# Kernel tuning notes

Hardware: AMD Instinct MI355X
Metric: run time of the kernel (lower is better)

Reference implementation:

```python
import jax, jax.numpy as jnp
import numpy as np
from jax import lax

B, C, T = 64, 122, 500
COUT, D, H, FF, L = 64, 128, 8, 256, 2
NSUB, NCLS = 13, 4
EPS = 1e-5


def _gelu(x):
    return jax.nn.gelu(x, approximate=False)  # torch nn.GELU default (erf)


def _bn(x, g, b, m, v):
    # eval-mode BatchNorm1d over channel dim of [N, C, T]
    scale = (g / jnp.sqrt(v + EPS))[None, :, None]
    return (x - m[None, :, None]) * scale + b[None, :, None]


def _ln(x, g, b):
    mu = x.mean(-1, keepdims=True)
    var = ((x - mu) ** 2).mean(-1, keepdims=True)
    return (x - mu) / jnp.sqrt(var + EPS) * g + b


def _conv1d(x, w, b, pad):
    y = lax.conv_general_dilated(x, w, (1,), [(pad, pad)], dimension_numbers=('NCH', 'OIH', 'NCH'))
    return y + b[None, :, None]


def forward(x, subject_ids, conv1_w, conv1_b, bn1_g, bn1_b, bn1_m, bn1_v,
            conv2_w, conv2_b, bn2_g, bn2_b, bn2_m, bn2_v,
            proj_w, proj_b, elec_emb,
            qkv_w, qkv_b, out_w, out_b, ln1_g, ln1_b,
            ff1_w, ff1_b, ff2_w, ff2_b, ln2_g, ln2_b,
            heads_w, heads_b):
    bsz = x.shape[0]
    h = x.reshape(bsz * C, 1, T)                               # [B*C, 1, T]
    h = _gelu(_bn(_conv1d(h, conv1_w, conv1_b, 4), bn1_g, bn1_b, bn1_m, bn1_v))
    h = h.reshape(bsz * C, COUT, T // 2, 2).max(-1)            # MaxPool1d(2)
    h = _gelu(_bn(_conv1d(h, conv2_w, conv2_b, 2), bn2_g, bn2_b, bn2_m, bn2_v))
    h = h.mean(-1)                                             # AdaptiveAvgPool1d(1)
    tok = h @ proj_w.T + proj_b                                # [B*C, D]
    tok = tok.reshape(bsz, C, D) + elec_emb[:, :C, :]
    dh = D // H
    inv_sqrt_dh = 1.0 / float(np.sqrt(dh))
    for l in range(L):  # post-norm TransformerEncoderLayer, gelu activation
        qkv = jnp.einsum('bsd,ed->bse', tok, qkv_w[l]) + qkv_b[l]
        q, k, v = jnp.split(qkv, 3, axis=-1)
        q = q.reshape(bsz, C, H, dh)
        k = k.reshape(bsz, C, H, dh)
        v = v.reshape(bsz, C, H, dh)
        att = jax.nn.softmax(jnp.einsum('bqhd,bkhd->bhqk', q, k) * inv_sqrt_dh, axis=-1)
        ctx = jnp.einsum('bhqk,bkhd->bqhd', att, v).reshape(bsz, C, D)
        tok = _ln(tok + ctx @ out_w[l].T + out_b[l], ln1_g[l], ln1_b[l])
        ff = _gelu(tok @ ff1_w[l].T + ff1_b[l]) @ ff2_w[l].T + ff2_b[l]
        tok = _ln(tok + ff, ln2_g[l], ln2_b[l])
    pooled = tok.mean(axis=1)                                  # [B, D]
    # per-subject head routing == gather subject's weight/bias, batched matvec
    hw = heads_w[subject_ids]                                  # [B, NCLS, D]
    hb = heads_b[subject_ids]                                  # [B, NCLS]
    return jnp.einsum('bd,bcd->bc', pooled, hw) + hb


def setup_inputs() -> dict:
    key = jax.random.key(0)
    ks = jax.random.split(key, 16)
    def n(i, shape, s=0.02):
        return jax.random.normal(ks[i], shape, jnp.float32) * s
    return {
        'x': jax.random.normal(ks[0], (B, C, T), jnp.float32),
        'subject_ids': jax.random.randint(ks[1], (B,), 0, NSUB),
        'conv1_w': n(2, (COUT, 1, 9), 0.3), 'conv1_b': jnp.zeros((COUT,), jnp.float32),
        'bn1_g': jnp.ones((COUT,), jnp.float32), 'bn1_b': jnp.zeros((COUT,), jnp.float32),
        'bn1_m': jnp.zeros((COUT,), jnp.float32), 'bn1_v': jnp.ones((COUT,), jnp.float32),
        'conv2_w': n(3, (COUT, COUT, 5), 0.05), 'conv2_b': jnp.zeros((COUT,), jnp.float32),
        'bn2_g': jnp.ones((COUT,), jnp.float32), 'bn2_b': jnp.zeros((COUT,), jnp.float32),
        'bn2_m': jnp.zeros((COUT,), jnp.float32), 'bn2_v': jnp.ones((COUT,), jnp.float32),
        'proj_w': n(4, (D, COUT), 0.05), 'proj_b': jnp.zeros((D,), jnp.float32),
        'elec_emb': n(5, (1, C, D), 0.02),
        'qkv_w': n(6, (L, 3 * D, D), 0.05), 'qkv_b': jnp.zeros((L, 3 * D), jnp.float32),
        'out_w': n(7, (L, D, D), 0.05), 'out_b': jnp.zeros((L, D), jnp.float32),
        'ln1_g': jnp.ones((L, D), jnp.float32), 'ln1_b': jnp.zeros((L, D), jnp.float32),
        'ff1_w': n(8, (L, FF, D), 0.05), 'ff1_b': jnp.zeros((L, FF), jnp.float32),
        'ff2_w': n(9, (L, D, FF), 0.05), 'ff2_b': jnp.zeros((L, D), jnp.float32),
        'ln2_g': jnp.ones((L, D), jnp.float32), 'ln2_b': jnp.zeros((L, D), jnp.float32),
        'heads_w': n(10, (NSUB, NCLS, D), 0.05), 'heads_b': jnp.zeros((NSUB, NCLS), jnp.float32),
    }


def reference(x, subject_ids, conv1_w, conv1_b, bn1_g, bn1_b, bn1_m, bn1_v,
              conv2_w, conv2_b, bn2_g, bn2_b, bn2_m, bn2_v,
              proj_w, proj_b, elec_emb,
              qkv_w, qkv_b, out_w, out_b, ln1_g, ln1_b,
              ff1_w, ff1_b, ff2_w, ff2_b, ln2_g, ln2_b,
              heads_w, heads_b):
    return forward(x, subject_ids, conv1_w, conv1_b, bn1_g, bn1_b, bn1_m, bn1_v,
                   conv2_w, conv2_b, bn2_g, bn2_b, bn2_m, bn2_v,
                   proj_w, proj_b, elec_emb,
                   qkv_w, qkv_b, out_w, out_b, ln1_g, ln1_b,
                   ff1_w, ff1_b, ff2_w, ff2_b, ln2_g, ln2_b,
                   heads_w, heads_b)
```

## Files before the change

kernel.cpp:

```cpp
#include <hip/hip_runtime.h>
#include <math.h>

#define BB 64
#define CC 122
#define TT 500
#define NCOUT 64
#define DD 128
#define HHEADS 8
#define FFDIM 256
#define NLAYER 2
#define EPS 1e-5f
#define SEQ (BB*CC)

#define WS_W2T     0u
#define WS_S1      20480u
#define WS_SH1     20544u
#define WS_S2      20608u
#define WS_SH2     20672u
#define WS_WBF     20736u
#define WS_TOK     151808u
#define WS_QKV     1151232u
#define WS_CTX     4149504u
#define WS_GTAB    6148352u
#define WS_W1S     6149376u

#define WB_QKV  0u
#define WB_OUT  98304u
#define WB_FF1  131072u
#define WB_FF2  196608u

typedef __attribute__((ext_vector_type(8))) short bf16x8;
typedef __attribute__((ext_vector_type(4))) float f32x4;

__device__ __forceinline__ unsigned short f2bf(float f) {
    unsigned int u = __float_as_uint(f);
    unsigned int r = u + 0x7FFFu + ((u >> 16) & 1u);
    return (unsigned short)(r >> 16);
}

__device__ __forceinline__ float gelu_fast(float x) {
    float z = fabsf(x) * 0.70710678118654752f;
    float t = __builtin_amdgcn_rcpf(fmaf(0.3275911f, z, 1.0f));
    float p = fmaf(fmaf(fmaf(fmaf(1.061405429f, t, -1.453152027f), t,
                             1.421413741f), t, -0.284496736f), t, 0.254829592f);
    float e = __expf(-z * z);
    float erf_abs = fmaf(-p * t, e, 1.0f);
    float erf_x = copysignf(erf_abs, x);
    return 0.5f * x * (1.0f + erf_x);
}

__device__ __forceinline__ float gelu_tab(float x, const float* __restrict__ gt) {
    float p = fmaf(x, 32.0f, 256.0f);
    p = fminf(fmaxf(p, 0.0f), 511.999f);
    int i = (int)p;
    float fr = p - (float)i;
    float2 gd = *(const float2*)&gt[2*i];
    return fmaf(fr, gd.y, gd.x);
}

__global__ void prep_kernel(const float* __restrict__ conv1_w, const float* __restrict__ conv1_b,
                            const float* __restrict__ bn1_g, const float* __restrict__ bn1_b,
                            const float* __restrict__ bn1_m, const float* __restrict__ bn1_v,
                            const float* __restrict__ conv2_w, const float* __restrict__ conv2_b,
                            const float* __restrict__ bn2_g, const float* __restrict__ bn2_b,
                            const float* __restrict__ bn2_m, const float* __restrict__ bn2_v,
                            const float* __restrict__ qkv_w, const float* __restrict__ out_w,
                            const float* __restrict__ ff1_w, const float* __restrict__ ff2_w,
                            float* __restrict__ ws) {
    int idx = blockIdx.x * blockDim.x + threadIdx.x;
    if (idx < 20480) {
        int ci = idx & 63; int co = (idx >> 6) & 63; int kk = idx >> 12;
        unsigned short* wt = (unsigned short*)(ws + WS_W2T);
        wt[idx] = f2bf(conv2_w[(co*64 + ci)*5 + kk]);
    } else if (idx < 20544) {
        int i = idx - 20480;
        float s = bn1_g[i] * rsqrtf(bn1_v[i] + EPS);
        ws[WS_S1 + i] = s;
        ws[WS_SH1 + i] = (conv1_b[i] - bn1_m[i]) * s + bn1_b[i];
    } else if (idx < 20608) {
        int i = idx - 20544;
        float s = bn2_g[i] * rsqrtf(bn2_v[i] + EPS);
        ws[WS_S2 + i] = s;
        ws[WS_SH2 + i] = (conv2_b[i] - bn2_m[i]) * s + bn2_b[i];
    } else if (idx < 282752) {
        int r = idx - 20608;
        unsigned short* wbf = (unsigned short*)(ws + WS_WBF);
        float v;
        if (r < 98304)       v = qkv_w[r];
        else if (r < 131072) v = out_w[r - 98304];
        else if (r < 196608) v = ff1_w[r - 131072];
        else                 v = ff2_w[r - 196608];
        wbf[r] = f2bf(v);
    } else if (idx < 283264) {
        int i = idx - 282752;
        float x0 = (i - 256) * 0.03125f;
        float x1 = x0 + 0.03125f;
        float g0 = 0.5f*x0*(1.0f + erff(x0*0.70710678118654752f));
        float g1 = 0.5f*x1*(1.0f + erff(x1*0.70710678118654752f));
        ws[WS_GTAB + 2*i]     = g0;
        ws[WS_GTAB + 2*i + 1] = g1 - g0;
    } else if (idx < 285312) {
        int i = idx - 283264;
        int co = i >> 5, k = i & 31;
        unsigned short* w1s = (unsigned short*)(ws + WS_W1S);
        float s = bn1_g[co] * rsqrtf(bn1_v[co] + EPS);
        w1s[i] = (k < 9) ? f2bf(conv1_w[co*9 + k] * s) : (unsigned short)0;
    }
}

__global__ __launch_bounds__(256, 4) void conv_kernel(const float* __restrict__ x,
            const float* __restrict__ proj_w, const float* __restrict__ proj_b,
            const float* __restrict__ elec,
            const float* __restrict__ wsr, float* __restrict__ tok) {
    __shared__ __align__(16) unsigned short h1s[264*64];
    __shared__ __align__(16) unsigned short xbf[544];
    __shared__ __align__(16) float gtab[1024];
    __shared__ float part[256];
    __shared__ float mean_l[64];
    int n = blockIdx.x;
    int c = n % CC;
    int tid = threadIdx.x;
    const float* xg = x + (size_t)n * TT;

    for (int i = tid; i < 544; i += 256) {
        unsigned short v = 0;
        if (i >= 4 && i < 504) v = f2bf(xg[i-4]);
        xbf[i] = v;
    }
    {
        const float4* gsrc = (const float4*)(wsr + WS_GTAB);
        float4* gdst = (float4*)gtab;
        if (tid < 256) gdst[tid] = gsrc[tid];
    }
    for (int idx = tid; idx < 14*64; idx += 256) {
        int rr = idx >> 6;
        int r = (rr < 2) ? rr : (rr - 2 + 252);
        h1s[r*64 + (idx & 63)] = 0;
    }
    __syncthreads();

    int lane = tid & 63;
    int w = tid >> 6;
    int ln15 = lane & 15, lg = lane >> 4;

    {
        const unsigned short* w1s = (const unsigned short*)(wsr + WS_W1S);
        bf16x8 b1f[4];
        float sh1v[4];
#pragma unroll
        for (int nt = 0; nt < 4; nt++) {
            int co = nt*16 + ln15;
            b1f[nt] = *(const bf16x8*)&w1s[co*32 + lg*8];
            sh1v[nt] = wsr[WS_SH1 + co];
        }
        bool km[8];
#pragma unroll
        for (int j = 0; j < 8; j++) km[j] = (lg*8 + j) < 9;

        for (int mi = 0; mi < 8; mi++) {
            int mt = w*8 + mi;
            int t = mt*16 + ln15;
            short e[8];
#pragma unroll
            for (int j = 0; j < 8; j++) {
                unsigned short vv = xbf[t + lg*8 + j];
                e[j] = km[j] ? (short)vv : (short)0;
            }
            bf16x8 af = {e[0],e[1],e[2],e[3],e[4],e[5],e[6],e[7]};
#pragma unroll
            for (int nt = 0; nt < 4; nt++) {
                f32x4 cacc = __builtin_amdgcn_mfma_f32_16x16x32_bf16(af, b1f[nt],
                                (f32x4){0.f,0.f,0.f,0.f}, 0, 0, 0);
                float g0 = gelu_tab(cacc[0] + sh1v[nt], gtab);
                float g1 = gelu_tab(cacc[1] + sh1v[nt], gtab);
                float g2 = gelu_tab(cacc[2] + sh1v[nt], gtab);
                float g3 = gelu_tab(cacc[3] + sh1v[nt], gtab);
                int tpA = mt*8 + lg*2;
                if (tpA < 250) {
                    int co = nt*16 + ln15;
                    int r = tpA + 2;
                    int cp = (co >> 3) ^ (r & 7);
                    h1s[r*64 + cp*8 + (co & 7)] = f2bf(fmaxf(g0, g1));
                    int r2 = r + 1;
                    int cp2 = (co >> 3) ^ (r2 & 7);
                    h1s[r2*64 + cp2*8 + (co & 7)] = f2bf(fmaxf(g2, g3));
                }
            }
        }
    }
    __syncthreads();

    const unsigned short* wt = (const unsigned short*)(wsr + WS_W2T);
    f32x4 acc[4][4];
#pragma unroll
    for (int mi = 0; mi < 4; mi++)
#pragma unroll
        for (int nt = 0; nt < 4; nt++) acc[mi][nt] = (f32x4){0.f, 0.f, 0.f, 0.f};

    const unsigned short* wbase = wt + ln15*64 + lg*8;
#pragma unroll
    for (int kk = 0; kk < 5; kk++) {
#pragma unroll
        for (int s = 0; s < 2; s++) {
            bf16x8 bfv[4];
#pragma unroll
            for (int nt = 0; nt < 4; nt++)
                bfv[nt] = *(const bf16x8*)(wbase + kk*4096 + nt*1024 + s*32);
#pragma unroll
            for (int mi = 0; mi < 4; mi++) {
                int r = (w*4 + mi)*16 + ln15 + kk;
                int cp = (s*4 + lg) ^ (r & 7);
                bf16x8 af = *(const bf16x8*)&h1s[r*64 + cp*8];
#pragma unroll
                for (int nt = 0; nt < 4; nt++)
                    acc[mi][nt] = __builtin_amdgcn_mfma_f32_16x16x32_bf16(af, bfv[nt], acc[mi][nt], 0, 0, 0);
            }
        }
    }

#pragma unroll
    for (int nt = 0; nt < 4; nt++) {
        int co2 = nt*16 + ln15;
        float sc = wsr[WS_S2 + co2], sh = wsr[WS_SH2 + co2];
        float p = 0.f;
#pragma unroll
        for (int mi = 0; mi < 4; mi++) {
            int tbase = (w*4 + mi)*16 + lg*4;
#pragma unroll
            for (int i = 0; i < 4; i++) {
                if (tbase + i < 250)
                    p += gelu_tab(fmaf(acc[mi][nt][i], sc, sh), gtab);
            }
        }
        p += __shfl_down(p, 32, 64);
        p += __shfl_down(p, 16, 64);
        if (lane < 16) part[w*64 + co2] = p;
    }
    __syncthreads();
    if (tid < 64) {
        mean_l[tid] = (part[tid] + part[64+tid] + part[128+tid] + part[192+tid]) * (1.0f/250.0f);
    }
    __syncthreads();

    if (tid < DD) {
        int d = tid;
        float a = proj_b[d] + elec[c*DD + d];
#pragma unroll 8
        for (int o = 0; o < 64; o++) a = fmaf(mean_l[o], proj_w[d*64 + o], a);
        tok[(size_t)n * DD + d] = a;
    }
}

template<int K>
__global__ __launch_bounds__(256) void mfma_gemm(const float* __restrict__ Aptr,
        const unsigned short* __restrict__ Bbf,
        const float* __restrict__ bias,
        float* __restrict__ Cptr, int ldC) {
    const int tid = threadIdx.x;
    const int m0 = blockIdx.x * 32;
    const int n0 = blockIdx.y * 128;
    __shared__ __align__(16) unsigned short As[32*K];

    const float* A = Aptr + (size_t)m0 * K;
    for (int i = tid; i < 8*K; i += 256) {
        int m = i / (K/4); int kq = (i - m*(K/4))*4;
        float4 v = *(const float4*)(A + m*K + kq);
        int cp = (kq >> 3) ^ (m & 15);
        short4 s4 = make_short4((short)f2bf(v.x), (short)f2bf(v.y),
                                (short)f2bf(v.z), (short)f2bf(v.w));
        *(short4*)&As[m*K + cp*8 + (kq & 7)] = s4;
    }
    __syncthreads();

    const int lane = tid & 63, w = tid >> 6;
    const int ln15 = lane & 15, lg = lane >> 4;
    f32x4 acc[2][2];
#pragma unroll
    for (int mi = 0; mi < 2; mi++)
#pragma unroll
        for (int ni = 0; ni < 2; ni++) acc[mi][ni] = (f32x4){0.f, 0.f, 0.f, 0.f};

    const unsigned short* Bb = Bbf + (size_t)n0 * K;
#pragma unroll
    for (int kt = 0; kt < K/32; kt++) {
        bf16x8 af[2], bfv[2];
#pragma unroll
        for (int mi = 0; mi < 2; mi++) {
            int m = mi*16 + ln15;
            int cp = (kt*4 + lg) ^ (m & 15);
            af[mi] = *(const bf16x8*)&As[m*K + cp*8];
        }
#pragma unroll
        for (int ni = 0; ni < 2; ni++) {
            int nn = (w*2 + ni)*16 + ln15;
            bfv[ni] = *(const bf16x8*)&Bb[(size_t)nn*K + kt*32 + lg*8];
        }
#pragma unroll
        for (int mi = 0; mi < 2; mi++)
#pragma unroll
            for (int ni = 0; ni < 2; ni++)
                acc[mi][ni] = __builtin_amdgcn_mfma_f32_16x16x32_bf16(af[mi], bfv[ni], acc[mi][ni], 0, 0, 0);
    }

#pragma unroll
    for (int mi = 0; mi < 2; mi++)
#pragma unroll
        for (int ni = 0; ni < 2; ni++) {
            int nloc = (w*2 + ni)*16 + ln15;
            int nn = n0 + nloc;
            float bn = bias[nn];
#pragma unroll
            for (int i = 0; i < 4; i++) {
                int ml = mi*16 + lg*4 + i;
                Cptr[(size_t)(m0 + ml)*ldC + nn] = acc[mi][ni][i] + bn;
            }
        }
}

__global__ __launch_bounds__(256) void layer_tail(const float* __restrict__ ctx,
        const unsigned short* __restrict__ outW, const float* __restrict__ outb,
        float* __restrict__ tok,
        const float* __restrict__ ln1g, const float* __restrict__ ln1b,
        const unsigned short* __restrict__ B1, const float* __restrict__ b1,
        const unsigned short* __restrict__ B2, const float* __restrict__ b2,
        const float* __restrict__ ln2g, const float* __restrict__ ln2b) {
    const int tid = threadIdx.x;
    const int m0 = blockIdx.x * 32;
    __shared__ __align__(16) unsigned short As[32*128];
    __shared__ __align__(16) unsigned short Hs[32*256];
    __shared__ float Cs[32*129];

    const float* A = ctx + (size_t)m0 * 128;
    for (int i = tid; i < 1024; i += 256) {
        int m = i >> 5; int kq = (i & 31) * 4;
        float4 v = *(const float4*)(A + m*128 + kq);
        int cp = (kq >> 3) ^ (m & 15);
        short4 s4 = make_short4((short)f2bf(v.x), (short)f2bf(v.y),
                                (short)f2bf(v.z), (short)f2bf(v.w));
        *(short4*)&As[m*128 + cp*8 + (kq & 7)] = s4;
    }
    __syncthreads();

    const int lane = tid & 63, w = tid >> 6;
    const int ln15 = lane & 15, lg = lane >> 4;

    {
        f32x4 acc[2][2];
#pragma unroll
        for (int mi = 0; mi < 2; mi++)
#pragma unroll
            for (int ni = 0; ni < 2; ni++) acc[mi][ni] = (f32x4){0.f, 0.f, 0.f, 0.f};
#pragma unroll
        for (int kt = 0; kt < 4; kt++) {
            bf16x8 af[2], bfv[2];
#pragma unroll
            for (int mi = 0; mi < 2; mi++) {
                int m = mi*16 + ln15;
                int cp = (kt*4 + lg) ^ (m & 15);
                af[mi] = *(const bf16x8*)&As[m*128 + cp*8];
            }
#pragma unroll
            for (int ni = 0; ni < 2; ni++) {
                int nn = (w*2 + ni)*16 + ln15;
                bfv[ni] = *(const bf16x8*)&outW[(size_t)nn*128 + kt*32 + lg*8];
            }
#pragma unroll
            for (int mi = 0; mi < 2; mi++)
#pragma unroll
                for (int ni = 0; ni < 2; ni++)
                    acc[mi][ni] = __builtin_amdgcn_mfma_f32_16x16x32_bf16(af[mi], bfv[ni], acc[mi][ni], 0, 0, 0);
        }
#pragma unroll
        for (int mi = 0; mi < 2; mi++)
#pragma unroll
            for (int ni = 0; ni < 2; ni++) {
                int nloc = (w*2 + ni)*16 + ln15;
                float bb = outb[nloc];
#pragma unroll
                for (int i = 0; i < 4; i++) {
                    int ml = mi*16 + lg*4 + i;
                    Cs[ml*129 + nloc] = acc[mi][ni][i] + bb + tok[(size_t)(m0 + ml)*128 + nloc];
                }
            }
    }
    __syncthreads();

    {
        int r = tid >> 3, sub = tid & 7;
        float s1 = 0.f, s2 = 0.f;
#pragma unroll
        for (int j = 0; j < 16; j++) {
            float vv = Cs[r*129 + sub*16 + j];
            s1 += vv; s2 += vv*vv;
        }
        s1 += __shfl_down(s1, 4, 64); s2 += __shfl_down(s2, 4, 64);
        s1 += __shfl_down(s1, 2, 64); s2 += __shfl_down(s2, 2, 64);
        s1 += __shfl_down(s1, 1, 64); s2 += __shfl_down(s2, 1, 64);
        int lb = lane & 56;
        s1 = __shfl(s1, lb, 64); s2 = __shfl(s2, lb, 64);
        float mu = s1 * (1.0f/128.0f);
        float var = s2 * (1.0f/128.0f) - mu*mu;
        float rstd = rsqrtf(var + EPS);
#pragma unroll
        for (int j = 0; j < 16; j++) {
            int nloc = sub*16 + j;
            float vv = (Cs[r*129 + nloc] - mu) * rstd * ln1g[nloc] + ln1b[nloc];
            Cs[r*129 + nloc] = vv;
            int cp = (nloc >> 3) ^ (r & 15);
            As[r*128 + cp*8 + (nloc & 7)] = f2bf(vv);
        }
    }
    __syncthreads();

    {
        f32x4 acc1[2][4];
#pragma unroll
        for (int mi = 0; mi < 2; mi++)
#pragma unroll
            for (int ni = 0; ni < 4; ni++) acc1[mi][ni] = (f32x4){0.f, 0.f, 0.f, 0.f};
#pragma unroll
        for (int kt = 0; kt < 4; kt++) {
            bf16x8 af[2];
#pragma unroll
            for (int mi = 0; mi < 2; mi++) {
                int m = mi*16 + ln15;
                int cp = (kt*4 + lg) ^ (m & 15);
                af[mi] = *(const bf16x8*)&As[m*128 + cp*8];
            }
#pragma unroll
            for (int ni = 0; ni < 4; ni++) {
                int nn = w*64 + ni*16 + ln15;
                bf16x8 bfv = *(const bf16x8*)&B1[(size_t)nn*128 + kt*32 + lg*8];
#pragma unroll
                for (int mi = 0; mi < 2; mi++)
                    acc1[mi][ni] = __builtin_amdgcn_mfma_f32_16x16x32_bf16(af[mi], bfv, acc1[mi][ni], 0, 0, 0);
            }
        }
#pragma unroll
        for (int ni = 0; ni < 4; ni++) {
            int nn = w*64 + ni*16 + ln15;
            float bb = b1[nn];
#pragma unroll
            for (int mi = 0; mi < 2; mi++)
#pragma unroll
                for (int i = 0; i < 4; i++) {
                    int m = mi*16 + lg*4 + i;
                    float v = gelu_fast(acc1[mi][ni][i] + bb);
                    int cp = ((nn >> 3) ^ (m & 15));
                    Hs[m*256 + cp*8 + (nn & 7)] = f2bf(v);
                }
        }
    }
    __syncthreads();

    {
        f32x4 acc2[2][2];
#pragma unroll
        for (int mi = 0; mi < 2; mi++)
#pragma unroll
            for (int ni = 0; ni < 2; ni++) acc2[mi][ni] = (f32x4){0.f, 0.f, 0.f, 0.f};
#pragma unroll
        for (int kt = 0; kt < 8; kt++) {
            bf16x8 af[2];
#pragma unroll
            for (int mi = 0; mi < 2; mi++) {
                int m = mi*16 + ln15;
                int cp = (kt*4 + lg) ^ (m & 15);
                af[mi] = *(const bf16x8*)&Hs[m*256 + cp*8];
            }
#pragma unroll
            for (int ni = 0; ni < 2; ni++) {
                int nn = (w*2 + ni)*16 + ln15;
                bf16x8 bfv = *(const bf16x8*)&B2[(size_t)nn*256 + kt*32 + lg*8];
#pragma unroll
                for (int mi = 0; mi < 2; mi++)
                    acc2[mi][ni] = __builtin_amdgcn_mfma_f32_16x16x32_bf16(af[mi], bfv, acc2[mi][ni], 0, 0, 0);
            }
        }
        __syncthreads();
#pragma unroll
        for (int mi = 0; mi < 2; mi++)
#pragma unroll
            for (int ni = 0; ni < 2; ni++) {
                int nloc = (w*2 + ni)*16 + ln15;
                float bb = b2[nloc];
#pragma unroll
                for (int i = 0; i < 4; i++) {
                    int ml = mi*16 + lg*4 + i;
                    Cs[ml*129 + nloc] = acc2[mi][ni][i] + bb + Cs[ml*129 + nloc];
                }
            }
    }
    __syncthreads();

    {
        int r = tid >> 3, sub = tid & 7;
        float s1 = 0.f, s2 = 0.f;
#pragma unroll
        for (int j = 0; j < 16; j++) {
            float vv = Cs[r*129 + sub*16 + j];
            s1 += vv; s2 += vv*vv;
        }
        s1 += __shfl_down(s1, 4, 64); s2 += __shfl_down(s2, 4, 64);
        s1 += __shfl_down(s1, 2, 64); s2 += __shfl_down(s2, 2, 64);
        s1 += __shfl_down(s1, 1, 64); s2 += __shfl_down(s2, 1, 64);
        int lb = lane & 56;
        s1 = __shfl(s1, lb, 64); s2 = __shfl(s2, lb, 64);
        float mu = s1 * (1.0f/128.0f);
        float var = s2 * (1.0f/128.0f) - mu*mu;
        float rstd = rsqrtf(var + EPS);
#pragma unroll
        for (int j = 0; j < 16; j++) {
            int nloc = sub*16 + j;
            float vv = (Cs[r*129 + nloc] - mu) * rstd * ln2g[nloc] + ln2b[nloc];
            tok[(size_t)(m0 + r)*128 + nloc] = vv;
        }
    }
}

__global__ __launch_bounds__(128) void attn_kernel(const float* __restrict__ qkv,
                                                   float* __restrict__ ctx) {
    __shared__ float qs[CC*16], ks[CC*16], vs[CC*16];
    int b = blockIdx.x >> 3, h = blockIdx.x & 7;
    int tid = threadIdx.x;
    const float* basep = qkv + (size_t)b*CC*384;
    for (int idx = tid; idx < CC*16; idx += 128) {
        int s = idx >> 4, d = idx & 15;
        qs[idx] = basep[s*384 +        h*16 + d];
        ks[idx] = basep[s*384 + 128 + h*16 + d];
        vs[idx] = basep[s*384 + 256 + h*16 + d];
    }
    __syncthreads();
    int i = tid;
    if (i < CC) {
        float q[16];
#pragma unroll
        for (int d = 0; d < 16; d++) q[d] = qs[i*16+d];
        float mx = -1e30f;
        for (int j = 0; j < CC; j++) {
            float s = 0.f;
#pragma unroll
            for (int d = 0; d < 16; d++) s = fmaf(q[d], ks[j*16+d], s);
            mx = fmaxf(mx, s * 0.25f);
        }
        float sum = 0.f;
        float acc[16];
#pragma unroll
        for (int d = 0; d < 16; d++) acc[d] = 0.f;
        for (int j = 0; j < CC; j++) {
            float s = 0.f;
#pragma unroll
            for (int d = 0; d < 16; d++) s = fmaf(q[d], ks[j*16+d], s);
            float e = __expf(s * 0.25f - mx);
            sum += e;
#pragma unroll
            for (int d = 0; d < 16; d++) acc[d] = fmaf(e, vs[j*16+d], acc[d]);
        }
        float r = __builtin_amdgcn_rcpf(sum);
        float* op = ctx + ((size_t)b*CC + i)*DD + h*16;
#pragma unroll
        for (int d = 0; d < 16; d++) op[d] = acc[d] * r;
    }
}

__global__ __launch_bounds__(128) void final_kernel(const float* __restrict__ tok,
        const int* __restrict__ sid,
        const float* __restrict__ hw, const float* __restrict__ hb,
        float* __restrict__ outp) {
    __shared__ float pool[DD];
    int b = blockIdx.x, tid = threadIdx.x;
    float s = 0.f;
    for (int c2 = 0; c2 < CC; c2++) s += tok[((size_t)b*CC + c2)*DD + tid];
    pool[tid] = s * (1.0f/(float)CC);
    __syncthreads();
    if (tid < 4) {
        int sb = sid[b];
        const float* w = hw + ((size_t)sb*4 + tid)*DD;
        float a = hb[sb*4 + tid];
#pragma unroll 8
        for (int d = 0; d < DD; d++) a = fmaf(pool[d], w[d], a);
        outp[b*4 + tid] = a;
    }
}

extern "C" void kernel_launch(void* const* d_in, const int* in_sizes, int n_in,
                              void* d_out, int out_size, void* d_ws, size_t ws_size,
                              hipStream_t stream) {
    const float* x       = (const float*)d_in[0];
    const int*   sid     = (const int*)  d_in[1];
    const float* conv1_w = (const float*)d_in[2];
    const float* conv1_b = (const float*)d_in[3];
    const float* bn1_g   = (const float*)d_in[4];
    const float* bn1_b   = (const float*)d_in[5];
    const float* bn1_m   = (const float*)d_in[6];
    const float* bn1_v   = (const float*)d_in[7];
    const float* conv2_w = (const float*)d_in[8];
    const float* conv2_b = (const float*)d_in[9];
    const float* bn2_g   = (const float*)d_in[10];
    const float* bn2_b   = (const float*)d_in[11];
    const float* bn2_m   = (const float*)d_in[12];
    const float* bn2_v   = (const float*)d_in[13];
    const float* proj_w  = (const float*)d_in[14];
    const float* proj_b  = (const float*)d_in[15];
    const float* elec    = (const float*)d_in[16];
    const float* qkv_w   = (const float*)d_in[17];
    const float* qkv_b   = (const float*)d_in[18];
    const float* out_w   = (const float*)d_in[19];
    const float* out_b   = (const float*)d_in[20];
    const float* ln1_g   = (const float*)d_in[21];
    const float* ln1_b   = (const float*)d_in[22];
    const float* ff1_w   = (const float*)d_in[23];
    const float* ff1_b   = (const float*)d_in[24];
    const float* ff2_w   = (const float*)d_in[25];
    const float* ff2_b   = (const float*)d_in[26];
    const float* ln2_g   = (const float*)d_in[27];
    const float* ln2_b   = (const float*)d_in[28];
    const float* heads_w = (const float*)d_in[29];
    const float* heads_b = (const float*)d_in[30];
    float* ws = (float*)d_ws;
    const unsigned short* wbf = (const unsigned short*)(ws + WS_WBF);

    prep_kernel<<<(285312 + 255)/256, 256, 0, stream>>>(
        conv1_w, conv1_b, bn1_g, bn1_b, bn1_m, bn1_v,
        conv2_w, conv2_b, bn2_g, bn2_b, bn2_m, bn2_v,
        qkv_w, out_w, ff1_w, ff2_w, ws);

    conv_kernel<<<SEQ, 256, 0, stream>>>(x, proj_w, proj_b, elec, ws, ws + WS_TOK);

    for (int l = 0; l < NLAYER; l++) {
        mfma_gemm<128><<<dim3(244,3), 256, 0, stream>>>(
            ws + WS_TOK, wbf + WB_QKV + l*49152, qkv_b + l*384,
            ws + WS_QKV, 384);
        attn_kernel<<<BB*HHEADS, 128, 0, stream>>>(ws + WS_QKV, ws + WS_CTX);
        layer_tail<<<244, 256, 0, stream>>>(
            ws + WS_CTX, wbf + WB_OUT + l*16384, out_b + l*128,
            ws + WS_TOK, ln1_g + l*128, ln1_b + l*128,
            wbf + WB_FF1 + l*32768, ff1_b + l*256,
            wbf + WB_FF2 + l*32768, ff2_b + l*128,
            ln2_g + l*128, ln2_b + l*128);
    }

    final_kernel<<<BB, 128, 0, stream>>>(ws + WS_TOK, sid, heads_w, heads_b, (float*)d_out);
}
```

Measured before the change: 485.9 us.

## Fuse MFMA attention into layer tail and store QKV as bf16 with transposed V

The scalar per-thread attention kernel is replaced by MFMA-based QK^T and PV computed inside the layer-tail kernel. Each block handles 32 query rows of one batch and runs the out-projection, LN1, FFN and LN2 in the same kernel. The QKV GEMM now writes bf16 Q/K and a transposed bf16 V, which removes the fp32 QKV and ctx round trips through global memory and one launch per layer. The conv input masking is also dropped, which relies on the padded conv1 weights being zero. The columns of V for keys 122..127 are never written and are read with zero probability weights, so leftover NaNs there could corrupt results.

```diff
diff --git a/kernel.cpp b/kernel.cpp
--- a/kernel.cpp
+++ b/kernel.cpp
@@ -19,10 +19,10 @@
 #define WS_SH2     20672u
 #define WS_WBF     20736u
 #define WS_TOK     151808u
-#define WS_QKV     1151232u
-#define WS_CTX     4149504u
-#define WS_GTAB    6148352u
-#define WS_W1S     6149376u
+#define WS_QKVB    1151232u
+#define WS_VTB     2150656u
+#define WS_GTAB    2674944u
+#define WS_W1S     2675968u
 
 #define WB_QKV  0u
 #define WB_OUT  98304u
@@ -153,19 +153,12 @@
             b1f[nt] = *(const bf16x8*)&w1s[co*32 + lg*8];
             sh1v[nt] = wsr[WS_SH1 + co];
         }
-        bool km[8];
-#pragma unroll
-        for (int j = 0; j < 8; j++) km[j] = (lg*8 + j) < 9;
-
         for (int mi = 0; mi < 8; mi++) {
             int mt = w*8 + mi;
             int t = mt*16 + ln15;
             short e[8];
 #pragma unroll
-            for (int j = 0; j < 8; j++) {
-                unsigned short vv = xbf[t + lg*8 + j];
-                e[j] = km[j] ? (short)vv : (short)0;
-            }
+            for (int j = 0; j < 8; j++) e[j] = (short)xbf[t + lg*8 + j];
             bf16x8 af = {e[0],e[1],e[2],e[3],e[4],e[5],e[6],e[7]};
 #pragma unroll
             for (int nt = 0; nt < 4; nt++) {
@@ -251,24 +244,25 @@
     }
 }
 
-template<int K>
-__global__ __launch_bounds__(256) void mfma_gemm(const float* __restrict__ Aptr,
+__global__ __launch_bounds__(256) void qkv_gemm(const float* __restrict__ Aptr,
         const unsigned short* __restrict__ Bbf,
         const float* __restrict__ bias,
-        float* __restrict__ Cptr, int ldC) {
+        unsigned short* __restrict__ qkvb,
+        unsigned short* __restrict__ vtb) {
     const int tid = threadIdx.x;
     const int m0 = blockIdx.x * 32;
-    const int n0 = blockIdx.y * 128;
-    __shared__ __align__(16) unsigned short As[32*K];
-
-    const float* A = Aptr + (size_t)m0 * K;
-    for (int i = tid; i < 8*K; i += 256) {
-        int m = i / (K/4); int kq = (i - m*(K/4))*4;
-        float4 v = *(const float4*)(A + m*K + kq);
+    const int y  = blockIdx.y;
+    const int n0 = y * 128;
+    __shared__ __align__(16) unsigned short As[32*128];
+
+    const float* A = Aptr + (size_t)m0 * 128;
+    for (int i = tid; i < 1024; i += 256) {
+        int m = i >> 5; int kq = (i & 31)*4;
+        float4 v = *(const float4*)(A + m*128 + kq);
         int cp = (kq >> 3) ^ (m & 15);
         short4 s4 = make_short4((short)f2bf(v.x), (short)f2bf(v.y),
                                 (short)f2bf(v.z), (short)f2bf(v.w));
-        *(short4*)&As[m*K + cp*8 + (kq & 7)] = s4;
+        *(short4*)&As[m*128 + cp*8 + (kq & 7)] = s4;
     }
     __syncthreads();
 
@@ -280,20 +274,20 @@
 #pragma unroll
         for (int ni = 0; ni < 2; ni++) acc[mi][ni] = (f32x4){0.f, 0.f, 0.f, 0.f};
 
-    const unsigned short* Bb = Bbf + (size_t)n0 * K;
-#pragma unroll
-    for (int kt = 0; kt < K/32; kt++) {
+    const unsigned short* Bb = Bbf + (size_t)n0 * 128;
+#pragma unroll
+    for (int kt = 0; kt < 4; kt++) {
         bf16x8 af[2], bfv[2];
 #pragma unroll
         for (int mi = 0; mi < 2; mi++) {
             int m = mi*16 + ln15;
             int cp = (kt*4 + lg) ^ (m & 15);
-            af[mi] = *(const bf16x8*)&As[m*K + cp*8];
+            af[mi] = *(const bf16x8*)&As[m*128 + cp*8];
         }
 #pragma unroll
         for (int ni = 0; ni < 2; ni++) {
             int nn = (w*2 + ni)*16 + ln15;
-            bfv[ni] = *(const bf16x8*)&Bb[(size_t)nn*K + kt*32 + lg*8];
+            bfv[ni] = *(const bf16x8*)&Bb[(size_t)nn*128 + kt*32 + lg*8];
         }
 #pragma unroll
         for (int mi = 0; mi < 2; mi++)
@@ -307,68 +301,161 @@
 #pragma unroll
         for (int ni = 0; ni < 2; ni++) {
             int nloc = (w*2 + ni)*16 + ln15;
-            int nn = n0 + nloc;
-            float bn = bias[nn];
+            float bb = bias[n0 + nloc];
 #pragma unroll
             for (int i = 0; i < 4; i++) {
                 int ml = mi*16 + lg*4 + i;
-                Cptr[(size_t)(m0 + ml)*ldC + nn] = acc[mi][ni][i] + bn;
-            }
-        }
-}
-
-__global__ __launch_bounds__(256) void layer_tail(const float* __restrict__ ctx,
+                int nrow = m0 + ml;
+                unsigned short us = f2bf(acc[mi][ni][i] + bb);
+                if (y < 2) {
+                    qkvb[(size_t)nrow*256 + n0 + nloc] = us;
+                } else {
+                    int bq = nrow / 122;
+                    int j  = nrow - bq*122;
+                    vtb[((size_t)(bq*128 + nloc))*128 + j] = us;
+                }
+            }
+        }
+}
+
+__global__ __launch_bounds__(256) void attn_tail(
+        const unsigned short* __restrict__ qkvb,
+        const unsigned short* __restrict__ vtb,
         const unsigned short* __restrict__ outW, const float* __restrict__ outb,
         float* __restrict__ tok,
         const float* __restrict__ ln1g, const float* __restrict__ ln1b,
         const unsigned short* __restrict__ B1, const float* __restrict__ b1,
         const unsigned short* __restrict__ B2, const float* __restrict__ b2,
         const float* __restrict__ ln2g, const float* __restrict__ ln2b) {
+    __shared__ float Cs[32*129];
+    __shared__ __align__(16) unsigned short Pregion[4*32*128];
+    __shared__ __align__(16) unsigned short ctxs[32*128];
+
     const int tid = threadIdx.x;
-    const int m0 = blockIdx.x * 32;
-    __shared__ __align__(16) unsigned short As[32*128];
-    __shared__ __align__(16) unsigned short Hs[32*256];
-    __shared__ float Cs[32*129];
-
-    const float* A = ctx + (size_t)m0 * 128;
-    for (int i = tid; i < 1024; i += 256) {
-        int m = i >> 5; int kq = (i & 31) * 4;
-        float4 v = *(const float4*)(A + m*128 + kq);
-        int cp = (kq >> 3) ^ (m & 15);
-        short4 s4 = make_short4((short)f2bf(v.x), (short)f2bf(v.y),
-                                (short)f2bf(v.z), (short)f2bf(v.w));
-        *(short4*)&As[m*128 + cp*8 + (kq & 7)] = s4;
-    }
-    __syncthreads();
-
+    const int blk = blockIdx.x;
+    const int b = blk >> 2, mq = blk & 3;
+    const int m0l = mq * 32;
     const int lane = tid & 63, w = tid >> 6;
     const int ln15 = lane & 15, lg = lane >> 4;
 
-    {
-        f32x4 acc[2][2];
-#pragma unroll
-        for (int mi = 0; mi < 2; mi++)
-#pragma unroll
-            for (int ni = 0; ni < 2; ni++) acc[mi][ni] = (f32x4){0.f, 0.f, 0.f, 0.f};
+    const unsigned short* qb = qkvb + (size_t)b * 122 * 256;
+    unsigned short* Pw = Pregion + w * 4096;
+
+#pragma unroll
+    for (int hs = 0; hs < 2; hs++) {
+        int h = w + hs*4;
+        bf16x8 af[2];
+#pragma unroll
+        for (int mi = 0; mi < 2; mi++) {
+            int mrow = m0l + mi*16 + ln15;
+            int gr = (mrow < 122) ? mrow : 121;
+            bf16x8 z = {0,0,0,0,0,0,0,0};
+            if (lg < 2) z = *(const bf16x8*)(qb + gr*256 + h*16 + lg*8);
+            af[mi] = z;
+        }
+        f32x4 S[2][8];
+#pragma unroll
+        for (int nt = 0; nt < 8; nt++) {
+            int j = nt*16 + ln15;
+            int gj = (j < 122) ? j : 121;
+            bf16x8 bv = {0,0,0,0,0,0,0,0};
+            if (lg < 2) bv = *(const bf16x8*)(qb + gj*256 + 128 + h*16 + lg*8);
+#pragma unroll
+            for (int mi = 0; mi < 2; mi++)
+                S[mi][nt] = __builtin_amdgcn_mfma_f32_16x16x32_bf16(af[mi], bv,
+                                (f32x4){0.f,0.f,0.f,0.f}, 0, 0, 0);
+        }
+        float sm[2][4];
+#pragma unroll
+        for (int mi = 0; mi < 2; mi++)
+#pragma unroll
+            for (int i = 0; i < 4; i++) {
+                float m_ = -1e30f;
+#pragma unroll
+                for (int nt = 0; nt < 8; nt++) {
+                    float v = S[mi][nt][i] * 0.25f;
+                    if (nt == 7 && ln15 >= 10) v = -1e30f;
+                    S[mi][nt][i] = v;
+                    m_ = fmaxf(m_, v);
+                }
+                m_ = fmaxf(m_, __shfl_xor(m_, 1, 64));
+                m_ = fmaxf(m_, __shfl_xor(m_, 2, 64));
+                m_ = fmaxf(m_, __shfl_xor(m_, 4, 64));
+                m_ = fmaxf(m_, __shfl_xor(m_, 8, 64));
+                float s_ = 0.f;
+#pragma unroll
+                for (int nt = 0; nt < 8; nt++) {
+                    float e = __expf(S[mi][nt][i] - m_);
+                    S[mi][nt][i] = e;
+                    s_ += e;
+                }
+                s_ += __shfl_xor(s_, 1, 64);
+                s_ += __shfl_xor(s_, 2, 64);
+                s_ += __shfl_xor(s_, 4, 64);
+                s_ += __shfl_xor(s_, 8, 64);
+                sm[mi][i] = s_;
+            }
+#pragma unroll
+        for (int mi = 0; mi < 2; mi++)
+#pragma unroll
+            for (int nt = 0; nt < 8; nt++)
+#pragma unroll
+                for (int i = 0; i < 4; i++) {
+                    int rp = mi*16 + lg*4 + i;
+                    int j = nt*16 + ln15;
+                    int cp = (j >> 3) ^ (rp & 15);
+                    Pw[rp*128 + cp*8 + (j & 7)] = f2bf(S[mi][nt][i]);
+                }
+        f32x4 cacc[2] = {(f32x4){0.f,0.f,0.f,0.f}, (f32x4){0.f,0.f,0.f,0.f}};
 #pragma unroll
         for (int kt = 0; kt < 4; kt++) {
-            bf16x8 af[2], bfv[2];
+            bf16x8 bv = *(const bf16x8*)(vtb + ((size_t)(b*128 + h*16 + ln15))*128 + kt*32 + lg*8);
 #pragma unroll
             for (int mi = 0; mi < 2; mi++) {
                 int m = mi*16 + ln15;
                 int cp = (kt*4 + lg) ^ (m & 15);
-                af[mi] = *(const bf16x8*)&As[m*128 + cp*8];
+                bf16x8 ap = *(const bf16x8*)&Pw[m*128 + cp*8];
+                cacc[mi] = __builtin_amdgcn_mfma_f32_16x16x32_bf16(ap, bv, cacc[mi], 0, 0, 0);
+            }
+        }
+#pragma unroll
+        for (int mi = 0; mi < 2; mi++)
+#pragma unroll
+            for (int i = 0; i < 4; i++) {
+                float inv = __builtin_amdgcn_rcpf(sm[mi][i]);
+                int rp = mi*16 + lg*4 + i;
+                int ccol = h*16 + ln15;
+                int cp = (ccol >> 3) ^ (rp & 15);
+                ctxs[rp*128 + cp*8 + (ccol & 7)] = f2bf(cacc[mi][i] * inv);
+            }
+    }
+    __syncthreads();
+
+    {
+        f32x4 acc[2][2];
+#pragma unroll
+        for (int mi = 0; mi < 2; mi++)
+#pragma unroll
+            for (int ni = 0; ni < 2; ni++) acc[mi][ni] = (f32x4){0.f,0.f,0.f,0.f};
+#pragma unroll
+        for (int kt = 0; kt < 4; kt++) {
+            bf16x8 afm[2], bv[2];
+#pragma unroll
+            for (int mi = 0; mi < 2; mi++) {
+                int m = mi*16 + ln15;
+                int cp = (kt*4 + lg) ^ (m & 15);
+                afm[mi] = *(const bf16x8*)&ctxs[m*128 + cp*8];
             }
 #pragma unroll
             for (int ni = 0; ni < 2; ni++) {
                 int nn = (w*2 + ni)*16 + ln15;
-                bfv[ni] = *(const bf16x8*)&outW[(size_t)nn*128 + kt*32 + lg*8];
+                bv[ni] = *(const bf16x8*)&outW[(size_t)nn*128 + kt*32 + lg*8];
             }
 #pragma unroll
             for (int mi = 0; mi < 2; mi++)
 #pragma unroll
                 for (int ni = 0; ni < 2; ni++)
-                    acc[mi][ni] = __builtin_amdgcn_mfma_f32_16x16x32_bf16(af[mi], bfv[ni], acc[mi][ni], 0, 0, 0);
+                    acc[mi][ni] = __builtin_amdgcn_mfma_f32_16x16x32_bf16(afm[mi], bv[ni], acc[mi][ni], 0, 0, 0);
         }
 #pragma unroll
         for (int mi = 0; mi < 2; mi++)
@@ -379,12 +466,16 @@
 #pragma unroll
                 for (int i = 0; i < 4; i++) {
                     int ml = mi*16 + lg*4 + i;
-                    Cs[ml*129 + nloc] = acc[mi][ni][i] + bb + tok[(size_t)(m0 + ml)*128 + nloc];
-                }
-            }
-    }
-    __syncthreads();
-
+                    int mrow = m0l + ml;
+                    int grow = b*122 + ((mrow < 122) ? mrow : 121);
+                    Cs[ml*129 + nloc] = acc[mi][ni][i] + bb + tok[(size_t)grow*128 + nloc];
+                }
+            }
+    }
+    __syncthreads();
+
+    unsigned short* ln1buf = Pregion;
+    unsigned short* Hs = Pregion + 4096;
     {
         int r = tid >> 3, sub = tid & 7;
         float s1 = 0.f, s2 = 0.f;
@@ -407,7 +498,7 @@
             float vv = (Cs[r*129 + nloc] - mu) * rstd * ln1g[nloc] + ln1b[nloc];
             Cs[r*129 + nloc] = vv;
             int cp = (nloc >> 3) ^ (r & 15);
-            As[r*128 + cp*8 + (nloc & 7)] = f2bf(vv);
+            ln1buf[r*128 + cp*8 + (nloc & 7)] = f2bf(vv);
         }
     }
     __syncthreads();
@@ -417,23 +508,23 @@
 #pragma unroll
         for (int mi = 0; mi < 2; mi++)
 #pragma unroll
-            for (int ni = 0; ni < 4; ni++) acc1[mi][ni] = (f32x4){0.f, 0.f, 0.f, 0.f};
+            for (int ni = 0; ni < 4; ni++) acc1[mi][ni] = (f32x4){0.f,0.f,0.f,0.f};
 #pragma unroll
         for (int kt = 0; kt < 4; kt++) {
-            bf16x8 af[2];
+            bf16x8 afm[2];
 #pragma unroll
             for (int mi = 0; mi < 2; mi++) {
                 int m = mi*16 + ln15;
                 int cp = (kt*4 + lg) ^ (m & 15);
-                af[mi] = *(const bf16x8*)&As[m*128 + cp*8];
+                afm[mi] = *(const bf16x8*)&ln1buf[m*128 + cp*8];
             }
 #pragma unroll
             for (int ni = 0; ni < 4; ni++) {
                 int nn = w*64 + ni*16 + ln15;
-                bf16x8 bfv = *(const bf16x8*)&B1[(size_t)nn*128 + kt*32 + lg*8];
+                bf16x8 bv = *(const bf16x8*)&B1[(size_t)nn*128 + kt*32 + lg*8];
 #pragma unroll
                 for (int mi = 0; mi < 2; mi++)
-                    acc1[mi][ni] = __builtin_amdgcn_mfma_f32_16x16x32_bf16(af[mi], bfv, acc1[mi][ni], 0, 0, 0);
+                    acc1[mi][ni] = __builtin_amdgcn_mfma_f32_16x16x32_bf16(afm[mi], bv, acc1[mi][ni], 0, 0, 0);
             }
         }
 #pragma unroll
@@ -446,7 +537,7 @@
                 for (int i = 0; i < 4; i++) {
                     int m = mi*16 + lg*4 + i;
                     float v = gelu_fast(acc1[mi][ni][i] + bb);
-                    int cp = ((nn >> 3) ^ (m & 15));
+                    int cp = (nn >> 3) ^ (m & 15);
                     Hs[m*256 + cp*8 + (nn & 7)] = f2bf(v);
                 }
         }
@@ -458,26 +549,25 @@
 #pragma unroll
         for (int mi = 0; mi < 2; mi++)
 #pragma unroll
-            for (int ni = 0; ni < 2; ni++) acc2[mi][ni] = (f32x4){0.f, 0.f, 0.f, 0.f};
+            for (int ni = 0; ni < 2; ni++) acc2[mi][ni] = (f32x4){0.f,0.f,0.f,0.f};
 #pragma unroll
         for (int kt = 0; kt < 8; kt++) {
-            bf16x8 af[2];
+            bf16x8 afm[2];
 #pragma unroll
             for (int mi = 0; mi < 2; mi++) {
                 int m = mi*16 + ln15;
                 int cp = (kt*4 + lg) ^ (m & 15);
-                af[mi] = *(const bf16x8*)&Hs[m*256 + cp*8];
+                afm[mi] = *(const bf16x8*)&Hs[m*256 + cp*8];
             }
 #pragma unroll
             for (int ni = 0; ni < 2; ni++) {
                 int nn = (w*2 + ni)*16 + ln15;
-                bf16x8 bfv = *(const bf16x8*)&B2[(size_t)nn*256 + kt*32 + lg*8];
+                bf16x8 bv = *(const bf16x8*)&B2[(size_t)nn*256 + kt*32 + lg*8];
 #pragma unroll
                 for (int mi = 0; mi < 2; mi++)
-                    acc2[mi][ni] = __builtin_amdgcn_mfma_f32_16x16x32_bf16(af[mi], bfv, acc2[mi][ni], 0, 0, 0);
-            }
-        }
-        __syncthreads();
+                    acc2[mi][ni] = __builtin_amdgcn_mfma_f32_16x16x32_bf16(afm[mi], bv, acc2[mi][ni], 0, 0, 0);
+            }
+        }
 #pragma unroll
         for (int mi = 0; mi < 2; mi++)
 #pragma unroll
@@ -509,57 +599,14 @@
         float mu = s1 * (1.0f/128.0f);
         float var = s2 * (1.0f/128.0f) - mu*mu;
         float rstd = rsqrtf(var + EPS);
-#pragma unroll
-        for (int j = 0; j < 16; j++) {
-            int nloc = sub*16 + j;
-            float vv = (Cs[r*129 + nloc] - mu) * rstd * ln2g[nloc] + ln2b[nloc];
-            tok[(size_t)(m0 + r)*128 + nloc] = vv;
-        }
-    }
-}
-
-__global__ __launch_bounds__(128) void attn_kernel(const float* __restrict__ qkv,
-                                                   float* __restrict__ ctx) {
-    __shared__ float qs[CC*16], ks[CC*16], vs[CC*16];
-    int b = blockIdx.x >> 3, h = blockIdx.x & 7;
-    int tid = threadIdx.x;
-    const float* basep = qkv + (size_t)b*CC*384;
-    for (int idx = tid; idx < CC*16; idx += 128) {
-        int s = idx >> 4, d = idx & 15;
-        qs[idx] = basep[s*384 +        h*16 + d];
-        ks[idx] = basep[s*384 + 128 + h*16 + d];
-        vs[idx] = basep[s*384 + 256 + h*16 + d];
-    }
-    __syncthreads();
-    int i = tid;
-    if (i < CC) {
-        float q[16];
-#pragma unroll
-        for (int d = 0; d < 16; d++) q[d] = qs[i*16+d];
-        float mx = -1e30f;
-        for (int j = 0; j < CC; j++) {
-            float s = 0.f;
-#pragma unroll
-            for (int d = 0; d < 16; d++) s = fmaf(q[d], ks[j*16+d], s);
-            mx = fmaxf(mx, s * 0.25f);
-        }
-        float sum = 0.f;
-        float acc[16];
-#pragma unroll
-        for (int d = 0; d < 16; d++) acc[d] = 0.f;
-        for (int j = 0; j < CC; j++) {
-            float s = 0.f;
-#pragma unroll
-            for (int d = 0; d < 16; d++) s = fmaf(q[d], ks[j*16+d], s);
-            float e = __expf(s * 0.25f - mx);
-            sum += e;
-#pragma unroll
-            for (int d = 0; d < 16; d++) acc[d] = fmaf(e, vs[j*16+d], acc[d]);
-        }
-        float r = __builtin_amdgcn_rcpf(sum);
-        float* op = ctx + ((size_t)b*CC + i)*DD + h*16;
-#pragma unroll
-        for (int d = 0; d < 16; d++) op[d] = acc[d] * r;
+        if (m0l + r < 122) {
+#pragma unroll
+            for (int j = 0; j < 16; j++) {
+                int nloc = sub*16 + j;
+                float vv = (Cs[r*129 + nloc] - mu) * rstd * ln2g[nloc] + ln2b[nloc];
+                tok[((size_t)(b*122 + m0l + r))*128 + nloc] = vv;
+            }
+        }
     }
 }
 
@@ -619,6 +666,8 @@
     const float* heads_b = (const float*)d_in[30];
     float* ws = (float*)d_ws;
     const unsigned short* wbf = (const unsigned short*)(ws + WS_WBF);
+    unsigned short* qkvb = (unsigned short*)(ws + WS_QKVB);
+    unsigned short* vtb  = (unsigned short*)(ws + WS_VTB);
 
     prep_kernel<<<(285312 + 255)/256, 256, 0, stream>>>(
         conv1_w, conv1_b, bn1_g, bn1_b, bn1_m, bn1_v,
@@ -628,12 +677,11 @@
     conv_kernel<<<SEQ, 256, 0, stream>>>(x, proj_w, proj_b, elec, ws, ws + WS_TOK);
 
     for (int l = 0; l < NLAYER; l++) {
-        mfma_gemm<128><<<dim3(244,3), 256, 0, stream>>>(
-            ws + WS_TOK, wbf + WB_QKV + l*49152, qkv_b + l*384,
-            ws + WS_QKV, 384);
-        attn_kernel<<<BB*HHEADS, 128, 0, stream>>>(ws + WS_QKV, ws + WS_CTX);
-        layer_tail<<<244, 256, 0, stream>>>(
-            ws + WS_CTX, wbf + WB_OUT + l*16384, out_b + l*128,
+        qkv_gemm<<<dim3(244,3), 256, 0, stream>>>(
+            ws + WS_TOK, wbf + WB_QKV + l*49152, qkv_b + l*384, qkvb, vtb);
+        attn_tail<<<BB*4, 256, 0, stream>>>(
+            qkvb, vtb,
+            wbf + WB_OUT + l*16384, out_b + l*128,
             ws + WS_TOK, ln1_g + l*128, ln1_b + l*128,
             wbf + WB_FF1 + l*32768, ff1_b + l*256,
             wbf + WB_FF2 + l*32768, ff2_b + l*128,
```

After: 434.5 us. 10.6% less time.
